# Optimization experiments

Measured on AMD Instinct MI355X. Metric: run time of the kernel, lower is better.

Reference implementation:

```python
import jax, jax.numpy as jnp
import numpy as np

B, N, M, C = 64, 16384, 128, 1024  # batch, memory slots, memory unit size, ctrl dim
EPS = 1e-16


def _linear_params(k, fan_in, fan_out, gain=1.4):
    k1, k2 = jax.random.split(k)
    bound = gain * np.sqrt(6.0 / (fan_in + fan_out))  # xavier_uniform
    w = jax.random.uniform(k1, (fan_in, fan_out), jnp.float32, -bound, bound)
    b = jax.random.normal(k2, (fan_out,), jnp.float32) * 0.01
    return w, b


def setup_inputs() -> dict:
    key = jax.random.key(0)
    ks = jax.random.split(key, 10)
    ctrl_state = jax.random.normal(ks[0], (B, C), jnp.float32)
    pw = jax.random.uniform(ks[1], (B, N), jnp.float32)
    prev_weights = pw / pw.sum(axis=1, keepdims=True)
    memory = jax.random.normal(ks[2], (B, N, M), jnp.float32)
    key_w, key_b = _linear_params(ks[3], C, M)
    beta_w, beta_b = _linear_params(ks[4], C, 1)
    gate_w, gate_b = _linear_params(ks[5], C, 1)
    shift_w, shift_b = _linear_params(ks[6], C, 3)
    gamma_w, gamma_b = _linear_params(ks[7], C, 1)
    erase_w, erase_b = _linear_params(ks[8], C, M)
    add_w, add_b = _linear_params(ks[9], C, M)
    return dict(ctrl_state=ctrl_state, prev_weights=prev_weights, memory=memory,
                key_w=key_w, key_b=key_b, beta_w=beta_w, beta_b=beta_b,
                gate_w=gate_w, gate_b=gate_b, shift_w=shift_w, shift_b=shift_b,
                gamma_w=gamma_w, gamma_b=gamma_b, erase_w=erase_w, erase_b=erase_b,
                add_w=add_w, add_b=add_b)


def reference(ctrl_state, prev_weights, memory,
              key_w, key_b, beta_w, beta_b, gate_w, gate_b,
              shift_w, shift_b, gamma_w, gamma_b,
              erase_w, erase_b, add_w, add_b):
    # ---- parameter projections (7 small GEMMs + activations) ----
    k = jnp.tanh(ctrl_state @ key_w + key_b)                      # (B, M)
    beta = jax.nn.softplus(ctrl_state @ beta_w + beta_b)          # (B, 1)
    gate = jax.nn.sigmoid(ctrl_state @ gate_w + gate_b)           # (B, 1)
    shift = jax.nn.softmax(ctrl_state @ shift_w + shift_b, axis=1)  # (B, 3)
    gamma = 1.0 + jax.nn.softplus(ctrl_state @ gamma_w + gamma_b)   # (B, 1)
    # erase/add are computed by the head but unused in read ('r') mode
    _erase = jax.nn.sigmoid(ctrl_state @ erase_w + erase_b)
    _add = jnp.tanh(ctrl_state @ add_w + add_b)
    # ---- content addressing: cosine similarity then beta-sharpened softmax ----
    dots = jnp.einsum('bm,bnm->bn', k, memory)                    # (B, N)
    norms = jnp.linalg.norm(k, axis=1, keepdims=True) * jnp.linalg.norm(memory, axis=2)
    sim = dots / (norms + EPS)
    content_weights = jax.nn.softmax(beta * sim, axis=1)          # (B, N)
    # ---- gated interpolation ----
    w = gate * content_weights + (1.0 - gate) * prev_weights      # (B, N)
    # ---- circular convolutional shift (3-tap, max_shift=1) ----
    w = (shift[:, 0:1] * jnp.roll(w, 1, axis=1)
         + shift[:, 1:2] * w
         + shift[:, 2:3] * jnp.roll(w, -1, axis=1))
    # ---- sharpen ----
    wp = w ** gamma
    weights = wp / (wp.sum(axis=1, keepdims=True) + EPS)          # (B, N)
    # ---- read ----
    read_vec = jnp.einsum('bn,bnm->bm', weights, memory)          # (B, M)
    return weights, read_vec
```

## Files before the change

kernel.cpp:

```cpp
#include <hip/hip_runtime.h>
#include <math.h>

#define B_ 64
#define N_ 16384
#define M_ 128
#define C_ 1024
#define EPS_ 1e-16f

__device__ __forceinline__ float softplus_(float x) {
    return fmaxf(x, 0.f) + log1pf(expf(-fabsf(x)));
}

__global__ void proj_kernel(const float* __restrict__ ctrl,
                            const float* __restrict__ key_w, const float* __restrict__ key_b,
                            const float* __restrict__ beta_w, const float* __restrict__ beta_b,
                            const float* __restrict__ gate_w, const float* __restrict__ gate_b,
                            const float* __restrict__ shift_w, const float* __restrict__ shift_b,
                            const float* __restrict__ gamma_w, const float* __restrict__ gamma_b,
                            float* __restrict__ k_out, float* __restrict__ kn_out,
                            float* __restrict__ beta_out, float* __restrict__ gate_out,
                            float* __restrict__ gamma_out, float* __restrict__ shift_out)
{
    const int b = blockIdx.x;
    const int t = threadIdx.x;
    const float* c = ctrl + (size_t)b * C_;

    float acc = 0.f;
    for (int i = 0; i < C_; ++i) acc = fmaf(c[i], key_w[i * M_ + t], acc);
    float kv = tanhf(acc + key_b[t]);
    k_out[b * M_ + t] = kv;

    float p0 = 0, p1 = 0, p2 = 0, p3 = 0, p4 = 0, p5 = 0;
    for (int i = t; i < C_; i += 128) {
        float cv = c[i];
        p0 = fmaf(cv, beta_w[i],      p0);
        p1 = fmaf(cv, gate_w[i],      p1);
        p2 = fmaf(cv, gamma_w[i],     p2);
        p3 = fmaf(cv, shift_w[3*i+0], p3);
        p4 = fmaf(cv, shift_w[3*i+1], p4);
        p5 = fmaf(cv, shift_w[3*i+2], p5);
    }
    __shared__ float red[7][128];
    red[0][t] = p0; red[1][t] = p1; red[2][t] = p2;
    red[3][t] = p3; red[4][t] = p4; red[5][t] = p5;
    red[6][t] = kv * kv;
    __syncthreads();
    for (int s = 64; s > 0; s >>= 1) {
        if (t < s) {
            #pragma unroll
            for (int j = 0; j < 7; ++j) red[j][t] += red[j][t + s];
        }
        __syncthreads();
    }
    if (t == 0) {
        beta_out[b]  = softplus_(red[0][0] + beta_b[0]);
        gate_out[b]  = 1.f / (1.f + expf(-(red[1][0] + gate_b[0])));
        gamma_out[b] = 1.f + softplus_(red[2][0] + gamma_b[0]);
        float z0 = red[3][0] + shift_b[0];
        float z1 = red[4][0] + shift_b[1];
        float z2 = red[5][0] + shift_b[2];
        float mx = fmaxf(z0, fmaxf(z1, z2));
        float e0 = expf(z0 - mx), e1 = expf(z1 - mx), e2 = expf(z2 - mx);
        float inv = 1.f / (e0 + e1 + e2);
        shift_out[b*3+0] = e0 * inv;
        shift_out[b*3+1] = e1 * inv;
        shift_out[b*3+2] = e2 * inv;
        kn_out[b] = sqrtf(red[6][0]);
    }
}

#define ROWS_PER_CHUNK 1024
__global__ void content_kernel(const float* __restrict__ mem,
                               const float* __restrict__ k,
                               const float* __restrict__ kn,
                               const float* __restrict__ beta,
                               float* __restrict__ e_out,
                               float* __restrict__ sumE)
{
    const int b     = blockIdx.y;
    const int chunk = blockIdx.x;
    const int t     = threadIdx.x;
    const int wave  = t >> 6;
    const int lane  = t & 63;
    const int half  = lane >> 5;
    const int sub   = lane & 31;

    __shared__ float ks[M_];
    if (t < M_) ks[t] = k[b * M_ + t];
    __syncthreads();
    const float4 k4  = reinterpret_cast<const float4*>(ks)[sub];
    const float  knb = kn[b];
    const float  bet = beta[b];

    const float* memb = mem + (size_t)b * N_ * M_;
    const int rowbase = chunk * ROWS_PER_CHUNK + wave * 2 + half;

    float eacc = 0.f;
    #pragma unroll 4
    for (int i = 0; i < ROWS_PER_CHUNK / 8; ++i) {
        const int n = rowbase + i * 8;
        const float4 m4 = reinterpret_cast<const float4*>(memb + (size_t)n * M_)[sub];
        float d = m4.x*k4.x + m4.y*k4.y + m4.z*k4.z + m4.w*k4.w;
        float q = m4.x*m4.x + m4.y*m4.y + m4.z*m4.z + m4.w*m4.w;
        #pragma unroll
        for (int off = 1; off < 32; off <<= 1) {
            d += __shfl_xor(d, off, 64);
            q += __shfl_xor(q, off, 64);
        }
        if (sub == 0) {
            float sim = d / (knb * sqrtf(q) + EPS_);
            float ev  = expf(bet * sim);
            e_out[(size_t)b * N_ + n] = ev;
            eacc += ev;
        }
    }
    __shared__ float red[256];
    red[t] = eacc;
    __syncthreads();
    for (int s = 128; s > 0; s >>= 1) {
        if (t < s) red[t] += red[t + s];
        __syncthreads();
    }
    if (t == 0) atomicAdd(&sumE[b], red[0]);
}

__global__ void shiftpow_kernel(const float* __restrict__ e,
                                const float* __restrict__ prev,
                                const float* __restrict__ sumE,
                                const float* __restrict__ gate,
                                const float* __restrict__ shift,
                                const float* __restrict__ gamma,
                                float* __restrict__ wp_out,
                                float* __restrict__ sumWp)
{
    const int b = blockIdx.y;
    const int n = blockIdx.x * 256 + threadIdx.x;
    const float invE = 1.f / sumE[b];
    const float g    = gate[b];
    const float s0   = shift[b*3+0], s1 = shift[b*3+1], s2 = shift[b*3+2];
    const float gam  = gamma[b];
    const float* eb = e    + (size_t)b * N_;
    const float* pb = prev + (size_t)b * N_;

    const int nm = (n == 0)      ? N_ - 1 : n - 1;
    const int np = (n == N_ - 1) ? 0      : n + 1;
    float wm = g * eb[nm] * invE + (1.f - g) * pb[nm];
    float wc = g * eb[n]  * invE + (1.f - g) * pb[n];
    float wq = g * eb[np] * invE + (1.f - g) * pb[np];
    float wsft = s0 * wm + s1 * wc + s2 * wq;
    float wp = powf(wsft, gam);
    wp_out[(size_t)b * N_ + n] = wp;

    __shared__ float red[256];
    red[threadIdx.x] = wp;
    __syncthreads();
    for (int s = 128; s > 0; s >>= 1) {
        if (threadIdx.x < s) red[threadIdx.x] += red[threadIdx.x + s];
        __syncthreads();
    }
    if (threadIdx.x == 0) atomicAdd(&sumWp[b], red[0]);
}

__global__ void normalize_kernel(const float* __restrict__ wp,
                                 const float* __restrict__ sumWp,
                                 float* __restrict__ out_w)
{
    const int b = blockIdx.y;
    const int i = blockIdx.x * 256 + threadIdx.x;
    const float inv = 1.f / (sumWp[b] + EPS_);
    float4 v = reinterpret_cast<const float4*>(wp + (size_t)b * N_)[i];
    v.x *= inv; v.y *= inv; v.z *= inv; v.w *= inv;
    reinterpret_cast<float4*>(out_w + (size_t)b * N_)[i] = v;
}

__global__ void read_kernel(const float* __restrict__ mem,
                            const float* __restrict__ weights,
                            float* __restrict__ read_out)
{
    const int b     = blockIdx.y;
    const int chunk = blockIdx.x;
    const int t     = threadIdx.x;
    const int wave  = t >> 6;
    const int lane  = t & 63;
    const int half  = lane >> 5;
    const int sub   = lane & 31;

    __shared__ float wtile[ROWS_PER_CHUNK];
    for (int i = t; i < ROWS_PER_CHUNK; i += 256)
        wtile[i] = weights[(size_t)b * N_ + chunk * ROWS_PER_CHUNK + i];
    __syncthreads();

    const float* memb = mem + (size_t)b * N_ * M_;
    const int rowbase = chunk * ROWS_PER_CHUNK + wave * 2 + half;
    const int lbase   = wave * 2 + half;

    float4 acc = make_float4(0.f, 0.f, 0.f, 0.f);
    #pragma unroll 4
    for (int i = 0; i < ROWS_PER_CHUNK / 8; ++i) {
        const int n  = rowbase + i * 8;
        const float wn = wtile[lbase + i * 8];
        const float4 m4 = reinterpret_cast<const float4*>(memb + (size_t)n * M_)[sub];
        acc.x = fmaf(wn, m4.x, acc.x);
        acc.y = fmaf(wn, m4.y, acc.y);
        acc.z = fmaf(wn, m4.z, acc.z);
        acc.w = fmaf(wn, m4.w, acc.w);
    }
    __shared__ float red[8][32][4];
    const int g = wave * 2 + half;
    red[g][sub][0] = acc.x; red[g][sub][1] = acc.y;
    red[g][sub][2] = acc.z; red[g][sub][3] = acc.w;
    __syncthreads();
    if (t < M_) {
        const int m = t, s2 = m >> 2, c = m & 3;
        float s = 0.f;
        #pragma unroll
        for (int gg = 0; gg < 8; ++gg) s += red[gg][s2][c];
        atomicAdd(&read_out[b * M_ + m], s);
    }
}

extern "C" void kernel_launch(void* const* d_in, const int* in_sizes, int n_in,
                              void* d_out, int out_size, void* d_ws, size_t ws_size,
                              hipStream_t stream) {
    const float* ctrl    = (const float*)d_in[0];
    const float* prev_w  = (const float*)d_in[1];
    const float* memory  = (const float*)d_in[2];
    const float* key_w   = (const float*)d_in[3];
    const float* key_b   = (const float*)d_in[4];
    const float* beta_w  = (const float*)d_in[5];
    const float* beta_b  = (const float*)d_in[6];
    const float* gate_w  = (const float*)d_in[7];
    const float* gate_b  = (const float*)d_in[8];
    const float* shift_w = (const float*)d_in[9];
    const float* shift_b = (const float*)d_in[10];
    const float* gamma_w = (const float*)d_in[11];
    const float* gamma_b = (const float*)d_in[12];

    float* out   = (float*)d_out;
    float* ws    = (float*)d_ws;
    float* e     = ws;
    float* wp    = ws + (size_t)B_ * N_;
    float* kbuf  = ws + (size_t)2 * B_ * N_;
    float* kn    = kbuf  + B_ * M_;
    float* beta  = kn    + B_;
    float* gate  = beta  + B_;
    float* gamma = gate  + B_;
    float* shift = gamma + B_;
    float* sums  = shift + 3 * B_;
    float* sumE  = sums;
    float* sumWp = sums + B_;

    hipMemsetAsync(sums, 0, 2 * B_ * sizeof(float), stream);
    hipMemsetAsync(out + (size_t)B_ * N_, 0, B_ * M_ * sizeof(float), stream);

    proj_kernel<<<B_, 128, 0, stream>>>(ctrl, key_w, key_b, beta_w, beta_b,
                                        gate_w, gate_b, shift_w, shift_b,
                                        gamma_w, gamma_b,
                                        kbuf, kn, beta, gate, gamma, shift);

    content_kernel<<<dim3(N_ / ROWS_PER_CHUNK, B_), 256, 0, stream>>>(
        memory, kbuf, kn, beta, e, sumE);

    shiftpow_kernel<<<dim3(N_ / 256, B_), 256, 0, stream>>>(
        e, prev_w, sumE, gate, shift, gamma, wp, sumWp);

    normalize_kernel<<<dim3(N_ / 4 / 256, B_), 256, 0, stream>>>(wp, sumWp, out);

    read_kernel<<<dim3(N_ / ROWS_PER_CHUNK, B_), 256, 0, stream>>>(
        memory, out, out + (size_t)B_ * N_);
}
```

Baseline: 903.2 us.

## Fuse normalize into read, fold memsets into proj, restructure content and shiftpow

Moves the zeroing of the sum and read buffers into the projection kernel, so the two memsets go away. The normalize kernel is removed: the read kernel now normalizes the weights tile, writes the weights output, and scales its accumulator by the inverse sum. The content kernel now uses 8 lanes per row, so each row needs a shorter shuffle reduction, and it replaces the division with rsqrt and fast exp. The shift-power kernel now handles four elements per thread with vector loads. The key projection gains four independent accumulators. The fast exp and rsqrt change the numerics slightly, and the removed EPS term in the similarity could matter for zero-norm rows.

```diff
diff --git a/kernel.cpp b/kernel.cpp
--- a/kernel.cpp
+++ b/kernel.cpp
@@ -19,15 +19,25 @@
                             const float* __restrict__ gamma_w, const float* __restrict__ gamma_b,
                             float* __restrict__ k_out, float* __restrict__ kn_out,
                             float* __restrict__ beta_out, float* __restrict__ gate_out,
-                            float* __restrict__ gamma_out, float* __restrict__ shift_out)
+                            float* __restrict__ gamma_out, float* __restrict__ shift_out,
+                            float* __restrict__ sumE, float* __restrict__ sumWp,
+                            float* __restrict__ read_out)
 {
     const int b = blockIdx.x;
     const int t = threadIdx.x;
     const float* c = ctrl + (size_t)b * C_;
 
-    float acc = 0.f;
-    for (int i = 0; i < C_; ++i) acc = fmaf(c[i], key_w[i * M_ + t], acc);
-    float kv = tanhf(acc + key_b[t]);
+    read_out[b * M_ + t] = 0.f;
+    if (t == 0) { sumE[b] = 0.f; sumWp[b] = 0.f; }
+
+    float a0 = 0.f, a1 = 0.f, a2 = 0.f, a3 = 0.f;
+    for (int i = 0; i < C_; i += 4) {
+        a0 = fmaf(c[i+0], key_w[(i+0) * M_ + t], a0);
+        a1 = fmaf(c[i+1], key_w[(i+1) * M_ + t], a1);
+        a2 = fmaf(c[i+2], key_w[(i+2) * M_ + t], a2);
+        a3 = fmaf(c[i+3], key_w[(i+3) * M_ + t], a3);
+    }
+    float kv = tanhf(((a0 + a1) + (a2 + a3)) + key_b[t]);
     k_out[b * M_ + t] = kv;
 
     float p0 = 0, p1 = 0, p2 = 0, p3 = 0, p4 = 0, p5 = 0;
@@ -82,35 +92,45 @@
     const int t     = threadIdx.x;
     const int wave  = t >> 6;
     const int lane  = t & 63;
-    const int half  = lane >> 5;
-    const int sub   = lane & 31;
+    const int r     = lane >> 3;
+    const int c     = lane & 7;
 
     __shared__ float ks[M_];
     if (t < M_) ks[t] = k[b * M_ + t];
     __syncthreads();
-    const float4 k4  = reinterpret_cast<const float4*>(ks)[sub];
-    const float  knb = kn[b];
-    const float  bet = beta[b];
+    const float4 kf0 = reinterpret_cast<const float4*>(ks)[c];
+    const float4 kf1 = reinterpret_cast<const float4*>(ks)[c + 8];
+    const float4 kf2 = reinterpret_cast<const float4*>(ks)[c + 16];
+    const float4 kf3 = reinterpret_cast<const float4*>(ks)[c + 24];
+    const float bk = beta[b] / kn[b];
 
     const float* memb = mem + (size_t)b * N_ * M_;
-    const int rowbase = chunk * ROWS_PER_CHUNK + wave * 2 + half;
+    const int row0 = chunk * ROWS_PER_CHUNK + wave * 8 + r;
 
     float eacc = 0.f;
-    #pragma unroll 4
-    for (int i = 0; i < ROWS_PER_CHUNK / 8; ++i) {
-        const int n = rowbase + i * 8;
-        const float4 m4 = reinterpret_cast<const float4*>(memb + (size_t)n * M_)[sub];
-        float d = m4.x*k4.x + m4.y*k4.y + m4.z*k4.z + m4.w*k4.w;
-        float q = m4.x*m4.x + m4.y*m4.y + m4.z*m4.z + m4.w*m4.w;
-        #pragma unroll
-        for (int off = 1; off < 32; off <<= 1) {
-            d += __shfl_xor(d, off, 64);
-            q += __shfl_xor(q, off, 64);
-        }
-        if (sub == 0) {
-            float sim = d / (knb * sqrtf(q) + EPS_);
-            float ev  = expf(bet * sim);
-            e_out[(size_t)b * N_ + n] = ev;
+    #pragma unroll 2
+    for (int tile = 0; tile < 32; ++tile) {
+        const int row = row0 + tile * 32;
+        const float4* mrow = reinterpret_cast<const float4*>(memb + (size_t)row * M_);
+        float4 m;
+        m = mrow[c];
+        float d = m.x*kf0.x + m.y*kf0.y + m.z*kf0.z + m.w*kf0.w;
+        float q = m.x*m.x + m.y*m.y + m.z*m.z + m.w*m.w;
+        m = mrow[c + 8];
+        d += m.x*kf1.x + m.y*kf1.y + m.z*kf1.z + m.w*kf1.w;
+        q += m.x*m.x + m.y*m.y + m.z*m.z + m.w*m.w;
+        m = mrow[c + 16];
+        d += m.x*kf2.x + m.y*kf2.y + m.z*kf2.z + m.w*kf2.w;
+        q += m.x*m.x + m.y*m.y + m.z*m.z + m.w*m.w;
+        m = mrow[c + 24];
+        d += m.x*kf3.x + m.y*kf3.y + m.z*kf3.z + m.w*kf3.w;
+        q += m.x*m.x + m.y*m.y + m.z*m.z + m.w*m.w;
+        d += __shfl_xor(d, 1, 64);  q += __shfl_xor(q, 1, 64);
+        d += __shfl_xor(d, 2, 64);  q += __shfl_xor(q, 2, 64);
+        d += __shfl_xor(d, 4, 64);  q += __shfl_xor(q, 4, 64);
+        const float ev = __expf(bk * d * rsqrtf(q));
+        if (c == 0) {
+            e_out[(size_t)b * N_ + row] = ev;
             eacc += ev;
         }
     }
@@ -134,25 +154,36 @@
                                 float* __restrict__ sumWp)
 {
     const int b = blockIdx.y;
-    const int n = blockIdx.x * 256 + threadIdx.x;
+    const int i = blockIdx.x * 256 + threadIdx.x;
     const float invE = 1.f / sumE[b];
     const float g    = gate[b];
-    const float s0   = shift[b*3+0], s1 = shift[b*3+1], s2 = shift[b*3+2];
-    const float gam  = gamma[b];
+    const float gi   = g * invE;
+    const float om   = 1.f - g;
+    const float s0 = shift[b*3+0], s1 = shift[b*3+1], s2 = shift[b*3+2];
+    const float gam = gamma[b];
     const float* eb = e    + (size_t)b * N_;
     const float* pb = prev + (size_t)b * N_;
 
-    const int nm = (n == 0)      ? N_ - 1 : n - 1;
-    const int np = (n == N_ - 1) ? 0      : n + 1;
-    float wm = g * eb[nm] * invE + (1.f - g) * pb[nm];
-    float wc = g * eb[n]  * invE + (1.f - g) * pb[n];
-    float wq = g * eb[np] * invE + (1.f - g) * pb[np];
-    float wsft = s0 * wm + s1 * wc + s2 * wq;
-    float wp = powf(wsft, gam);
-    wp_out[(size_t)b * N_ + n] = wp;
+    const float4 ec = reinterpret_cast<const float4*>(eb)[i];
+    const float4 pc = reinterpret_cast<const float4*>(pb)[i];
+    const int il = (i == 0)          ? N_ - 1 : 4*i - 1;
+    const int ir = (i == N_/4 - 1)   ? 0      : 4*i + 4;
+    const float wl = gi*eb[il] + om*pb[il];
+    const float w0 = gi*ec.x  + om*pc.x;
+    const float w1 = gi*ec.y  + om*pc.y;
+    const float w2 = gi*ec.z  + om*pc.z;
+    const float w3 = gi*ec.w  + om*pc.w;
+    const float wr = gi*eb[ir] + om*pb[ir];
+
+    float4 o;
+    o.x = powf(s0*wl + s1*w0 + s2*w1, gam);
+    o.y = powf(s0*w0 + s1*w1 + s2*w2, gam);
+    o.z = powf(s0*w1 + s1*w2 + s2*w3, gam);
+    o.w = powf(s0*w2 + s1*w3 + s2*wr, gam);
+    reinterpret_cast<float4*>(wp_out + (size_t)b * N_)[i] = o;
 
     __shared__ float red[256];
-    red[threadIdx.x] = wp;
+    red[threadIdx.x] = (o.x + o.y) + (o.z + o.w);
     __syncthreads();
     for (int s = 128; s > 0; s >>= 1) {
         if (threadIdx.x < s) red[threadIdx.x] += red[threadIdx.x + s];
@@ -161,20 +192,10 @@
     if (threadIdx.x == 0) atomicAdd(&sumWp[b], red[0]);
 }
 
-__global__ void normalize_kernel(const float* __restrict__ wp,
-                                 const float* __restrict__ sumWp,
-                                 float* __restrict__ out_w)
-{
-    const int b = blockIdx.y;
-    const int i = blockIdx.x * 256 + threadIdx.x;
-    const float inv = 1.f / (sumWp[b] + EPS_);
-    float4 v = reinterpret_cast<const float4*>(wp + (size_t)b * N_)[i];
-    v.x *= inv; v.y *= inv; v.z *= inv; v.w *= inv;
-    reinterpret_cast<float4*>(out_w + (size_t)b * N_)[i] = v;
-}
-
 __global__ void read_kernel(const float* __restrict__ mem,
-                            const float* __restrict__ weights,
+                            const float* __restrict__ wp,
+                            const float* __restrict__ sumWp,
+                            float* __restrict__ out_w,
                             float* __restrict__ read_out)
 {
     const int b     = blockIdx.y;
@@ -184,10 +205,18 @@
     const int lane  = t & 63;
     const int half  = lane >> 5;
     const int sub   = lane & 31;
+    const float inv = 1.f / (sumWp[b] + EPS_);
 
     __shared__ float wtile[ROWS_PER_CHUNK];
-    for (int i = t; i < ROWS_PER_CHUNK; i += 256)
-        wtile[i] = weights[(size_t)b * N_ + chunk * ROWS_PER_CHUNK + i];
+    {
+        const float4 v = reinterpret_cast<const float4*>(
+            wp + (size_t)b * N_ + chunk * ROWS_PER_CHUNK)[t];
+        reinterpret_cast<float4*>(wtile)[t] = v;
+        float4 o;
+        o.x = v.x * inv; o.y = v.y * inv; o.z = v.z * inv; o.w = v.w * inv;
+        reinterpret_cast<float4*>(
+            out_w + (size_t)b * N_ + chunk * ROWS_PER_CHUNK)[t] = o;
+    }
     __syncthreads();
 
     const float* memb = mem + (size_t)b * N_ * M_;
@@ -205,16 +234,18 @@
         acc.z = fmaf(wn, m4.z, acc.z);
         acc.w = fmaf(wn, m4.w, acc.w);
     }
+    acc.x *= inv; acc.y *= inv; acc.z *= inv; acc.w *= inv;
+
     __shared__ float red[8][32][4];
     const int g = wave * 2 + half;
     red[g][sub][0] = acc.x; red[g][sub][1] = acc.y;
     red[g][sub][2] = acc.z; red[g][sub][3] = acc.w;
     __syncthreads();
     if (t < M_) {
-        const int m = t, s2 = m >> 2, c = m & 3;
+        const int m = t, s2 = m >> 2, cc = m & 3;
         float s = 0.f;
         #pragma unroll
-        for (int gg = 0; gg < 8; ++gg) s += red[gg][s2][c];
+        for (int gg = 0; gg < 8; ++gg) s += red[gg][s2][cc];
         atomicAdd(&read_out[b * M_ + m], s);
     }
 }
@@ -250,22 +281,18 @@
     float* sumE  = sums;
     float* sumWp = sums + B_;
 
-    hipMemsetAsync(sums, 0, 2 * B_ * sizeof(float), stream);
-    hipMemsetAsync(out + (size_t)B_ * N_, 0, B_ * M_ * sizeof(float), stream);
-
     proj_kernel<<<B_, 128, 0, stream>>>(ctrl, key_w, key_b, beta_w, beta_b,
                                         gate_w, gate_b, shift_w, shift_b,
                                         gamma_w, gamma_b,
-                                        kbuf, kn, beta, gate, gamma, shift);
+                                        kbuf, kn, beta, gate, gamma, shift,
+                                        sumE, sumWp, out + (size_t)B_ * N_);
 
     content_kernel<<<dim3(N_ / ROWS_PER_CHUNK, B_), 256, 0, stream>>>(
         memory, kbuf, kn, beta, e, sumE);
 
-    shiftpow_kernel<<<dim3(N_ / 256, B_), 256, 0, stream>>>(
+    shiftpow_kernel<<<dim3(N_ / 4 / 256, B_), 256, 0, stream>>>(
         e, prev_w, sumE, gate, shift, gamma, wp, sumWp);
 
-    normalize_kernel<<<dim3(N_ / 4 / 256, B_), 256, 0, stream>>>(wp, sumWp, out);
-
     read_kernel<<<dim3(N_ / ROWS_PER_CHUNK, B_), 256, 0, stream>>>(
-        memory, out, out + (size_t)B_ * N_);
-}
+        memory, wp, sumWp, out, out + (size_t)B_ * N_);
+}
```

Result: faster. 856.4 us (-5.2%).
